# Kernel optimization log

Hardware: AMD Instinct MI355X
Metric: run time of the kernel (lower is better)

Reference implementation:

```python
import jax, jax.numpy as jnp
import numpy as np
import math

B, L, D_IN, H, N, NL, D_OUT = 16, 4096, 64, 256, 32, 4, 10
EPS = 1e-5


def setup_inputs() -> dict:
    key = jax.random.key(0)
    ks = jax.random.split(key, 16)
    inp = {}
    inp['x'] = jax.random.normal(ks[0], (B, L, D_IN), dtype=jnp.float32)
    inp['enc_w'] = jax.random.normal(ks[1], (H, D_IN), dtype=jnp.float32) / math.sqrt(D_IN)
    inp['enc_b'] = jax.random.normal(ks[2], (H,), dtype=jnp.float32) * 0.01
    # log_dt uniform in [log(1e-3), log(1e-1)] as in S4D init
    inp['log_dt'] = jax.random.uniform(ks[3], (NL, H), dtype=jnp.float32,
                                       minval=math.log(1e-3), maxval=math.log(1e-1))
    inp['log_A_real'] = jnp.full((NL, H, N), math.log(0.5), dtype=jnp.float32)
    inp['A_imag'] = jnp.broadcast_to(math.pi * jnp.arange(N, dtype=jnp.float32), (NL, H, N)).copy()
    inp['C_re'] = jax.random.normal(ks[4], (NL, H, N), dtype=jnp.float32)
    inp['C_im'] = jax.random.normal(ks[5], (NL, H, N), dtype=jnp.float32)
    inp['D'] = jax.random.normal(ks[6], (NL, H), dtype=jnp.float32)
    inp['out_w'] = jax.random.normal(ks[7], (NL, 2 * H, H), dtype=jnp.float32) / math.sqrt(H)
    inp['out_b'] = jax.random.normal(ks[8], (NL, 2 * H), dtype=jnp.float32) * 0.01
    inp['ln_w'] = jnp.ones((NL, H), dtype=jnp.float32)
    inp['ln_b'] = jnp.zeros((NL, H), dtype=jnp.float32)
    inp['dec_w'] = jax.random.normal(ks[9], (D_OUT, H), dtype=jnp.float32) / math.sqrt(H)
    inp['dec_b'] = jax.random.normal(ks[10], (D_OUT,), dtype=jnp.float32) * 0.01
    return inp


def _s4d_kernel(log_dt, log_A_real, A_imag, C_re, C_im, length):
    # log_dt: (H,), others: (H, N). Returns real conv kernel (H, length).
    dt = jnp.exp(log_dt)[:, None]                       # (H, 1)
    A = -jnp.exp(log_A_real) + 1j * A_imag              # (H, N), Re(A) < 0
    dtA = A * dt                                        # (H, N)
    C = (C_re + 1j * C_im) * (jnp.expm1(dtA)) / A       # ZOH-style scaling
    t = jnp.arange(length, dtype=jnp.float32)
    vand = jnp.exp(dtA[:, :, None] * t)                 # (H, N, L) Vandermonde
    K = 2.0 * jnp.real(jnp.einsum('hn,hnl->hl', C, vand))
    return K


def _fft_conv(u, k):
    # u: (B, H, L), k: (H, L) -> causal circular-padded conv, (B, H, L)
    length = u.shape[-1]
    k_f = jnp.fft.rfft(k, n=2 * length)                 # (H, L+1)
    u_f = jnp.fft.rfft(u, n=2 * length)                 # (B, H, L+1)
    return jnp.fft.irfft(u_f * k_f[None], n=2 * length)[..., :length]


def _layernorm_channels(x, w, b):
    # x: (B, H, L), normalize over channel dim H
    mu = jnp.mean(x, axis=1, keepdims=True)
    var = jnp.var(x, axis=1, keepdims=True)
    return (x - mu) * jax.lax.rsqrt(var + EPS) * w[None, :, None] + b[None, :, None]


def reference(x, enc_w, enc_b, log_dt, log_A_real, A_imag, C_re, C_im, D,
              out_w, out_b, ln_w, ln_b, dec_w, dec_b):
    # encoder: (B, L, d_input) -> (B, L, H), then transpose -> (B, H, L)
    h = jnp.einsum('bli,hi->blh', x, enc_w) + enc_b
    h = jnp.swapaxes(h, -1, -2)                         # (B, H, L)
    length = h.shape[-1]
    for i in range(NL):
        z = h
        K = _s4d_kernel(log_dt[i], log_A_real[i], A_imag[i], C_re[i], C_im[i], length)
        y = _fft_conv(z, K) + z * D[i][None, :, None]   # SSM conv + skip
        y = jax.nn.gelu(y)
        # position-wise 1x1 conv to 2H, then GLU over channel dim
        g = jnp.einsum('bhl,gh->bgl', y, out_w[i]) + out_b[i][None, :, None]
        g1, g2 = jnp.split(g, 2, axis=1)
        y = g1 * jax.nn.sigmoid(g2)
        h = y + h                                       # residual (dropout=0)
        h = _layernorm_channels(h, ln_w[i], ln_b[i])    # post-norm
    h = jnp.swapaxes(h, -1, -2)                         # (B, L, H)
    return jnp.einsum('blh,oh->blo', h, dec_w) + dec_b
```

## Files before the change

### kernel.cpp

```cpp
#include <hip/hip_runtime.h>
#include <hip/hip_fp16.h>

#define B_   16
#define L_   4096
#define DIN  64
#define H_   256
#define N_   32
#define NL_  4
#define DOUT 10
#define CH_  32
#define T_   128

#define GAS const __attribute__((address_space(1)))
#define LAS __attribute__((address_space(3)))

typedef _Float16 half8 __attribute__((ext_vector_type(8)));
typedef _Float16 half4 __attribute__((ext_vector_type(4)));
typedef float f32x4 __attribute__((ext_vector_type(4)));

__device__ __forceinline__ float gelu_f(float v) {
    float t3  = v * v * v;
    float arg = 0.7978845608028654f * fmaf(0.044715f, t3, v);
    float e   = __expf(2.f * arg);
    float th  = 1.f - 2.f / (e + 1.f);
    return 0.5f * v * (1.f + th);
}

__global__ __launch_bounds__(256) void gen_k(
    const float* __restrict__ log_dt, const float* __restrict__ log_A_real,
    const float* __restrict__ A_imag, const float* __restrict__ C_re, const float* __restrict__ C_im,
    const float* __restrict__ Dp,
    _Float16* __restrict__ Wv, _Float16* __restrict__ Vt, _Float16* __restrict__ G,
    float* __restrict__ wtr, float* __restrict__ wti)
{
    __shared__ float sxr[N_], sxi[N_], scr[N_], sci[N_], skd[T_];
    int ih = blockIdx.x;
    int t  = threadIdx.x;
    if (t < N_) {
        int n = t;
        float dt  = expf(log_dt[ih]);
        float Are = -expf(log_A_real[ih * N_ + n]);
        float Aim = A_imag[ih * N_ + n];
        float xr = dt * Are, xi = dt * Aim;
        float ex = expf(xr), cy = cosf(xi), sy = sinf(xi);
        float sh = sinf(0.5f * xi);
        float em_re = expm1f(xr) * cy - 2.f * sh * sh;
        float em_im = ex * sy;
        float inv = 1.f / (Are * Are + Aim * Aim);
        float qr = (em_re * Are + em_im * Aim) * inv;
        float qi = (em_im * Are - em_re * Aim) * inv;
        float crv = C_re[ih * N_ + n], civ = C_im[ih * N_ + n];
        sxr[n] = xr; sxi[n] = xi;
        scr[n] = 2.f * (crv * qr - civ * qi);
        sci[n] = 2.f * (crv * qi + civ * qr);
        float txr = 128.f * xr, txi = 128.f * xi;
        float exT = expf(txr);
        wtr[ih * N_ + n] = exT * cosf(txi);
        wti[ih * N_ + n] = exT * sinf(txi);
    }
    __syncthreads();
    if (t <= T_) {
        int d = t;
        float fd = (float)d;
        float kd = 0.f;
        for (int n = 0; n < N_; n++) {
            float ar = expf(fd * sxr[n]);
            float ang = fd * sxi[n];
            float wdr = ar * cosf(ang), wdi = ar * sinf(ang);
            if (d < T_) {
                kd = fmaf(scr[n], wdr, kd);
                kd = fmaf(-sci[n], wdi, kd);
                Wv[((size_t)ih * 64 + 2 * n) * T_ + (127 - d)]     = (_Float16)wdr;
                Wv[((size_t)ih * 64 + 2 * n + 1) * T_ + (127 - d)] = (_Float16)wdi;
            }
            if (d >= 1) {
                float vr = scr[n] * wdr - sci[n] * wdi;
                float vi = scr[n] * wdi + sci[n] * wdr;
                Vt[((size_t)ih * T_ + (d - 1)) * 64 + 2 * n]     = (_Float16)vr;
                Vt[((size_t)ih * T_ + (d - 1)) * 64 + 2 * n + 1] = (_Float16)(-vi);
            }
        }
        if (d < T_) skd[d] = kd;
    }
    __syncthreads();
    if (t < T_) {
        float v = skd[127 - t];
        if (t == 127) v += Dp[ih];
        G[(size_t)ih * 256 + t]       = (_Float16)v;
        G[(size_t)ih * 256 + 128 + t] = (_Float16)0.f;
    }
}

__global__ __launch_bounds__(256) void prep_k(
    const float* __restrict__ w, _Float16* __restrict__ w16,
    const float* __restrict__ dw, _Float16* __restrict__ dwp)
{
    int bx = blockIdx.x;
    int t  = threadIdx.x;
    if (bx < (NL_ * 2 * H_ * H_) / 256) {
        int idx = bx * 256 + t;
        w16[idx] = (_Float16)w[idx];
    } else {
#pragma unroll
        for (int j = 0; j < 16; j++) {
            int idx = j * 256 + t;
            dwp[idx] = (idx < DOUT * H_) ? (_Float16)dw[idx] : (_Float16)0.f;
        }
    }
}

__global__ __launch_bounds__(256) void encoder_k(
    const float* __restrict__ x, const float* __restrict__ ew,
    const float* __restrict__ eb, _Float16* __restrict__ z16)
{
    __shared__ _Float16 smem[35840];
    _Float16* xs  = smem;
    _Float16* ews = smem + 128 * 72;
    _Float16* ot  = smem;
    int b  = blockIdx.y;
    int l0 = blockIdx.x << 7;
    int t  = threadIdx.x;
#pragma unroll
    for (int j = 0; j < 8; j++) {
        int idx = j * 256 + t;
        int l = idx >> 4, i4 = (idx & 15) * 4;
        float4 v = *(const float4*)(x + ((size_t)(b * L_ + l0 + l)) * DIN + i4);
        _Float16 c[4] = {(_Float16)v.x, (_Float16)v.y, (_Float16)v.z, (_Float16)v.w};
        *(uint2*)&xs[l * 72 + i4] = *(uint2*)c;
    }
#pragma unroll
    for (int j = 0; j < 16; j++) {
        int idx = j * 256 + t;
        int h = idx >> 4, i4 = (idx & 15) * 4;
        float4 v = *(const float4*)(ew + h * 64 + i4);
        _Float16 c[4] = {(_Float16)v.x, (_Float16)v.y, (_Float16)v.z, (_Float16)v.w};
        *(uint2*)&ews[h * 72 + i4] = *(uint2*)c;
    }
    __syncthreads();
    int lane = t & 63, wid = t >> 6;
    int l15 = lane & 15, quad = lane >> 4;
    f32x4 acc[4][8];
#pragma unroll
    for (int mt = 0; mt < 4; mt++)
#pragma unroll
        for (int nt = 0; nt < 8; nt++) acc[mt][nt] = (f32x4){0.f,0.f,0.f,0.f};
#pragma unroll
    for (int ks = 0; ks < 2; ks++) {
        int kk = ks * 32 + quad * 8;
        half8 a[4], bb[8];
#pragma unroll
        for (int mt = 0; mt < 4; mt++)
            a[mt] = *(const half8*)&ews[(wid * 64 + mt * 16 + l15) * 72 + kk];
#pragma unroll
        for (int nt = 0; nt < 8; nt++)
            bb[nt] = *(const half8*)&xs[(nt * 16 + l15) * 72 + kk];
#pragma unroll
        for (int mt = 0; mt < 4; mt++)
#pragma unroll
            for (int nt = 0; nt < 8; nt++)
                acc[mt][nt] = __builtin_amdgcn_mfma_f32_16x16x32_f16(a[mt], bb[nt], acc[mt][nt], 0, 0, 0);
    }
    __syncthreads();
#pragma unroll
    for (int mt = 0; mt < 4; mt++) {
        int hb = wid * 64 + mt * 16 + quad * 4;
        float b0 = eb[hb], b1 = eb[hb + 1], b2 = eb[hb + 2], b3 = eb[hb + 3];
#pragma unroll
        for (int nt = 0; nt < 8; nt++) {
            int l = nt * 16 + l15;
            ot[(hb + 0) * 136 + l] = (_Float16)(acc[mt][nt][0] + b0);
            ot[(hb + 1) * 136 + l] = (_Float16)(acc[mt][nt][1] + b1);
            ot[(hb + 2) * 136 + l] = (_Float16)(acc[mt][nt][2] + b2);
            ot[(hb + 3) * 136 + l] = (_Float16)(acc[mt][nt][3] + b3);
        }
    }
    __syncthreads();
#pragma unroll
    for (int p = 0; p < 16; p++) {
        int row = p * 16 + (t >> 4), seg = t & 15;
        uint4 v = *(uint4*)&ot[row * 136 + seg * 8];
        *(uint4*)(z16 + ((size_t)(b * H_ + row)) * L_ + l0 + seg * 8) = v;
    }
}

__global__ __launch_bounds__(256, 4) void conv2_k(
    const _Float16* __restrict__ z16, const _Float16* __restrict__ G,
    const _Float16* __restrict__ Vt, const _Float16* __restrict__ Wv,
    const float* __restrict__ wtr, const float* __restrict__ wti,
    _Float16* __restrict__ y16)
{
    __shared__ _Float16 zT[64][136];
    __shared__ _Float16 Ff[64][72];
    __shared__ _Float16 Gs[256];
    int h = blockIdx.x, rb = blockIdx.y;
    int t = threadIdx.x;
    int b0 = rb * 2;
#pragma unroll
    for (int q = 0; q < 4; q++) {
        int idx = q * 256 + t;
        int brow = idx >> 9;
        int e = (idx & 511) * 8;
        uint4 v = *(const uint4*)(z16 + ((size_t)((b0 + brow) * H_ + h)) * L_ + e);
        int c = e >> 7, jj = e & 127;
        *(uint4*)&zT[brow * 32 + c][jj] = v;
    }
    Gs[t] = G[(size_t)h * 256 + t];
    __syncthreads();
    int lane = t & 63, w = t >> 6;
    int l15 = lane & 15, quad = lane >> 4;
    {
        int brow = w & 1, mhalf = w >> 1;
        f32x4 facc[2][2];
#pragma unroll
        for (int mt = 0; mt < 2; mt++) {
            facc[mt][0] = (f32x4){0.f,0.f,0.f,0.f};
            facc[mt][1] = (f32x4){0.f,0.f,0.f,0.f};
        }
        const _Float16* wvb = Wv + (size_t)h * 64 * T_;
#pragma unroll
        for (int ks = 0; ks < 4; ks++) {
            int kk = ks * 32 + quad * 8;
            half8 bf0 = *(const half8*)&zT[brow * 32 + l15][kk];
            half8 bf1 = *(const half8*)&zT[brow * 32 + 16 + l15][kk];
#pragma unroll
            for (int mt = 0; mt < 2; mt++) {
                half8 a = *(const half8*)(wvb + (size_t)((mhalf * 2 + mt) * 16 + l15) * T_ + kk);
                facc[mt][0] = __builtin_amdgcn_mfma_f32_16x16x32_f16(a, bf0, facc[mt][0], 0, 0, 0);
                facc[mt][1] = __builtin_amdgcn_mfma_f32_16x16x32_f16(a, bf1, facc[mt][1], 0, 0, 0);
            }
        }
#pragma unroll
        for (int mt = 0; mt < 2; mt++)
#pragma unroll
            for (int nt = 0; nt < 2; nt++) {
                int cr = brow * 32 + nt * 16 + l15;
                int cc = (mhalf * 2 + mt) * 16 + quad * 4;
#pragma unroll
                for (int r = 0; r < 4; r++)
                    Ff[cr][cc + r] = (_Float16)facc[mt][nt][r];
            }
    }
    __syncthreads();
    if (w < 2 && lane < 32) {
        int n = lane;
        float wr = wtr[h * N_ + n], wi = wti[h * N_ + n];
        float cr = 0.f, ci = 0.f;
        for (int c = 0; c < CH_; c++) {
            float fr = (float)Ff[w * 32 + c][2 * n];
            float fi = (float)Ff[w * 32 + c][2 * n + 1];
            Ff[w * 32 + c][2 * n]     = (_Float16)cr;
            Ff[w * 32 + c][2 * n + 1] = (_Float16)ci;
            float nr = fmaf(wr, cr, fr);
            nr = fmaf(-wi, ci, nr);
            float ni = fmaf(wi, cr, fi);
            ni = fmaf(wr, ci, ni);
            cr = nr; ci = ni;
        }
    }
    __syncthreads();
    f32x4 acc[2][4];
#pragma unroll
    for (int mt = 0; mt < 2; mt++)
#pragma unroll
        for (int nt = 0; nt < 4; nt++) acc[mt][nt] = (f32x4){0.f,0.f,0.f,0.f};
#pragma unroll
    for (int ks = 0; ks < 4; ks++) {
        int kk = ks * 32 + quad * 8;
        int base0 = 127 - (w * 32 + l15) + kk;
        int base1 = base0 - 16;
        half8 a0, a1;
#pragma unroll
        for (int j = 0; j < 8; j++) { a0[j] = Gs[base0 + j]; a1[j] = Gs[base1 + j]; }
#pragma unroll
        for (int nt = 0; nt < 4; nt++) {
            half8 bf = *(const half8*)&zT[nt * 16 + l15][kk];
            acc[0][nt] = __builtin_amdgcn_mfma_f32_16x16x32_f16(a0, bf, acc[0][nt], 0, 0, 0);
            acc[1][nt] = __builtin_amdgcn_mfma_f32_16x16x32_f16(a1, bf, acc[1][nt], 0, 0, 0);
        }
    }
    const _Float16* vb = Vt + (size_t)h * T_ * 64;
#pragma unroll
    for (int ks = 0; ks < 2; ks++) {
        int kk = ks * 32 + quad * 8;
        half8 a0 = *(const half8*)(vb + ((size_t)(w * 32 + l15)) * 64 + kk);
        half8 a1 = *(const half8*)(vb + ((size_t)(w * 32 + 16 + l15)) * 64 + kk);
#pragma unroll
        for (int nt = 0; nt < 4; nt++) {
            half8 bf = *(const half8*)&Ff[nt * 16 + l15][kk];
            acc[0][nt] = __builtin_amdgcn_mfma_f32_16x16x32_f16(a0, bf, acc[0][nt], 0, 0, 0);
            acc[1][nt] = __builtin_amdgcn_mfma_f32_16x16x32_f16(a1, bf, acc[1][nt], 0, 0, 0);
        }
    }
    __syncthreads();
#pragma unroll
    for (int mt = 0; mt < 2; mt++)
#pragma unroll
        for (int nt = 0; nt < 4; nt++) {
            int r = nt * 16 + l15;
            int tt0 = w * 32 + mt * 16 + quad * 4;
            _Float16 o[4];
#pragma unroll
            for (int rr = 0; rr < 4; rr++) o[rr] = (_Float16)gelu_f(acc[mt][nt][rr]);
            *(uint2*)&zT[r][tt0] = *(uint2*)o;
        }
    __syncthreads();
#pragma unroll
    for (int q = 0; q < 4; q++) {
        int idx = q * 256 + t;
        int brow = idx >> 9;
        int e = (idx & 511) * 8;
        int c = e >> 7, jj = e & 127;
        uint4 v = *(uint4*)&zT[brow * 32 + c][jj];
        *(uint4*)(y16 + ((size_t)((b0 + brow) * H_ + h)) * L_ + e) = v;
    }
}

__global__ __launch_bounds__(256, 2) void glu_k(
    const _Float16* __restrict__ W, const _Float16* __restrict__ y16,
    const float* __restrict__ outb, const float* __restrict__ lnw,
    const float* __restrict__ lnb, _Float16* __restrict__ z16)
{
    __shared__ __align__(16) _Float16 yT_u[64 * 266];
    __shared__ __align__(16) _Float16 zs[256 * 64];
    __shared__ float red[2][4][64];
    __shared__ float mus[64], rss[64];
    _Float16* yT = yT_u;
    _Float16* us = yT_u;
    int b  = blockIdx.y;
    int l0 = blockIdx.x << 6;
    int t  = threadIdx.x;
    int lane = t & 63, wid = t >> 6;
    int l15 = lane & 15, quad = lane >> 4;
    {
        const uint4* src = (const uint4*)(y16 + ((size_t)(b * H_ + t)) * L_ + l0);
        uint4 v[8];
#pragma unroll
        for (int j = 0; j < 8; j++) v[j] = src[j];
        {
            int rsub = lane >> 3, csub = (lane & 7) * 8;
#pragma unroll
            for (int q = 0; q < 8; q++) {
                int ch = wid * 64 + q * 8 + rsub;
                const _Float16* gp = z16 + ((size_t)(b * H_ + ch)) * L_ + l0 + csub;
                __builtin_amdgcn_global_load_lds((GAS unsigned*)(const void*)gp,
                                                 (LAS unsigned*)(void*)&zs[(wid * 64 + q * 8) * 64],
                                                 16, 0, 0);
            }
        }
        const _Float16* hv = (const _Float16*)v;
#pragma unroll
        for (int j = 0; j < 64; j++) yT[j * 266 + t] = hv[j];
    }
    __syncthreads();
    f32x4 acc[8][4];
#pragma unroll
    for (int mt = 0; mt < 8; mt++)
#pragma unroll
        for (int nt = 0; nt < 4; nt++) acc[mt][nt] = (f32x4){0.f,0.f,0.f,0.f};
#pragma unroll
    for (int ks = 0; ks < 8; ks++) {
        int kk = ks * 32 + quad * 8;
        half8 bf[4];
#pragma unroll
        for (int nt = 0; nt < 4; nt++) bf[nt] = *(const half8*)&yT[(nt * 16 + l15) * 266 + kk];
#pragma unroll
        for (int mt = 0; mt < 8; mt++) {
            int row = (mt >> 2) * 256 + wid * 64 + (mt & 3) * 16 + l15;
            half8 a = *(const half8*)(W + (size_t)row * H_ + kk);
#pragma unroll
            for (int nt = 0; nt < 4; nt++)
                acc[mt][nt] = __builtin_amdgcn_mfma_f32_16x16x32_f16(a, bf[nt], acc[mt][nt], 0, 0, 0);
        }
    }
    __syncthreads();
#pragma unroll
    for (int mt = 0; mt < 4; mt++) {
        int chb = wid * 64 + mt * 16 + quad * 4;
        float4 ob1 = *(const float4*)(outb + chb);
        float4 ob2 = *(const float4*)(outb + 256 + chb);
        const float* o1 = (const float*)&ob1;
        const float* o2 = (const float*)&ob2;
#pragma unroll
        for (int nt = 0; nt < 4; nt++) {
            int l = nt * 16 + l15;
#pragma unroll
            for (int r = 0; r < 4; r++) {
                float g1 = acc[mt][nt][r] + o1[r];
                float g2 = acc[mt + 4][nt][r] + o2[r];
                float sg = 1.f / (1.f + __expf(-g2));
                us[(chb + r) * 66 + l] = (_Float16)(g1 * sg);
            }
        }
    }
    __syncthreads();
    int lr = t & 63, grp = t >> 6;
    float s1 = 0.f, s2 = 0.f;
    for (int j = 0; j < 64; j++) {
        int ch = grp * 64 + j;
        float uu = (float)us[ch * 66 + lr] + (float)zs[ch * 64 + lr];
        us[ch * 66 + lr] = (_Float16)uu;
        s1 += uu; s2 = fmaf(uu, uu, s2);
    }
    red[0][grp][lr] = s1; red[1][grp][lr] = s2;
    __syncthreads();
    if (t < 64) {
        float a = red[0][0][t] + red[0][1][t] + red[0][2][t] + red[0][3][t];
        float q = red[1][0][t] + red[1][1][t] + red[1][2][t] + red[1][3][t];
        float mu  = a * (1.f / 256.f);
        float var = q * (1.f / 256.f) - mu * mu;
        mus[t] = mu; rss[t] = rsqrtf(var + 1e-5f);
    }
    __syncthreads();
    int lg = (t & 15) * 4, ch0 = t >> 4;
    float mu4[4], rs4[4];
#pragma unroll
    for (int i = 0; i < 4; i++) { mu4[i] = mus[lg + i]; rs4[i] = rss[lg + i]; }
#pragma unroll
    for (int j = 0; j < 16; j++) {
        int ch = ch0 + 16 * j;
        float wv = lnw[ch], bv = lnb[ch];
        _Float16 o4[4];
#pragma unroll
        for (int i = 0; i < 4; i++) {
            float vv = ((float)us[ch * 66 + lg + i] - mu4[i]) * rs4[i] * wv + bv;
            o4[i] = (_Float16)vv;
        }
        *(uint2*)(z16 + ((size_t)(b * H_ + ch)) * L_ + l0 + lg) = *(uint2*)o4;
    }
}

__global__ __launch_bounds__(256) void decoder_k(
    const _Float16* __restrict__ z16, const _Float16* __restrict__ dwp,
    const float* __restrict__ db, float* __restrict__ out)
{
    __shared__ _Float16 zT[128][268];
    int b  = blockIdx.y;
    int l0 = blockIdx.x << 7;
    int t  = threadIdx.x;
#pragma unroll 8
    for (int j = 0; j < 64; j++) {
        int idx = j * 256 + t;
        int h = idx >> 6, lp = idx & 63;
        unsigned v = *(const unsigned*)(z16 + ((size_t)(b * H_ + h)) * L_ + l0 + lp * 2);
        union { unsigned u; _Float16 f[2]; } c; c.u = v;
        zT[lp * 2][h]     = c.f[0];
        zT[lp * 2 + 1][h] = c.f[1];
    }
    __syncthreads();
    int lane = t & 63, wid = t >> 6;
    int l15 = lane & 15, quad = lane >> 4;
    f32x4 acc[2];
    acc[0] = (f32x4){0.f,0.f,0.f,0.f};
    acc[1] = (f32x4){0.f,0.f,0.f,0.f};
#pragma unroll
    for (int ks = 0; ks < 8; ks++) {
        int kk = ks * 32 + quad * 8;
        half8 a = *(const half8*)(dwp + l15 * 256 + kk);
#pragma unroll
        for (int nt = 0; nt < 2; nt++) {
            int l = (wid * 2 + nt) * 16 + l15;
            half4 lo = *(const half4*)&zT[l][kk];
            half4 hi = *(const half4*)&zT[l][kk + 4];
            half8 bf;
#pragma unroll
            for (int j = 0; j < 4; j++) { bf[j] = lo[j]; bf[j + 4] = hi[j]; }
            acc[nt] = __builtin_amdgcn_mfma_f32_16x16x32_f16(a, bf, acc[nt], 0, 0, 0);
        }
    }
    int o0 = quad * 4;
#pragma unroll
    for (int nt = 0; nt < 2; nt++) {
        int l = (wid * 2 + nt) * 16 + l15;
        float* op = out + ((size_t)(b * L_ + l0 + l)) * DOUT;
#pragma unroll
        for (int r = 0; r < 4; r++) {
            int o = o0 + r;
            if (o < DOUT) op[o] = acc[nt][r] + db[o];
        }
    }
}

extern "C" void kernel_launch(void* const* d_in, const int* in_sizes, int n_in,
                              void* d_out, int out_size, void* d_ws, size_t ws_size,
                              hipStream_t stream)
{
    (void)in_sizes; (void)n_in; (void)out_size; (void)ws_size;
    const float* x          = (const float*)d_in[0];
    const float* enc_w      = (const float*)d_in[1];
    const float* enc_b      = (const float*)d_in[2];
    const float* log_dt     = (const float*)d_in[3];
    const float* log_A_real = (const float*)d_in[4];
    const float* A_imag     = (const float*)d_in[5];
    const float* C_re       = (const float*)d_in[6];
    const float* C_im       = (const float*)d_in[7];
    const float* Dp         = (const float*)d_in[8];
    const float* out_w      = (const float*)d_in[9];
    const float* out_b      = (const float*)d_in[10];
    const float* ln_w       = (const float*)d_in[11];
    const float* ln_b       = (const float*)d_in[12];
    const float* dec_w      = (const float*)d_in[13];
    const float* dec_b      = (const float*)d_in[14];
    float* outp = (float*)d_out;

    char* ws = (char*)d_ws;
    _Float16* z16 = (_Float16*)ws;   ws += (size_t)B_ * H_ * L_ * 2;
    _Float16* y16 = (_Float16*)ws;   ws += (size_t)B_ * H_ * L_ * 2;
    _Float16* Wv = (_Float16*)ws;    ws += (size_t)NL_ * H_ * 64 * T_ * 2;
    _Float16* Vt = (_Float16*)ws;    ws += (size_t)NL_ * H_ * T_ * 64 * 2;
    _Float16* G  = (_Float16*)ws;    ws += (size_t)NL_ * H_ * 256 * 2;
    size_t tb = (size_t)NL_ * H_ * N_;
    float* wtr = (float*)ws; ws += tb * 4;
    float* wti = (float*)ws; ws += tb * 4;
    _Float16* W16 = (_Float16*)ws; ws += (size_t)NL_ * 2 * H_ * H_ * 2;
    _Float16* dwp = (_Float16*)ws; ws += (size_t)16 * H_ * 2;

    gen_k<<<NL_ * H_, 256, 0, stream>>>(log_dt, log_A_real, A_imag, C_re, C_im, Dp,
                                        Wv, Vt, G, wtr, wti);
    prep_k<<<(NL_ * 2 * H_ * H_) / 256 + 1, 256, 0, stream>>>(out_w, W16, dec_w, dwp);
    encoder_k<<<dim3(L_ / 128, B_), 256, 0, stream>>>(x, enc_w, enc_b, z16);
    for (int i = 0; i < NL_; i++) {
        size_t th = (size_t)i * H_;
        conv2_k<<<dim3(H_, B_ / 2), 256, 0, stream>>>(z16, G + th * 256, Vt + th * T_ * 64,
                                                      Wv + th * 64 * T_, wtr + th * N_, wti + th * N_,
                                                      y16);
        glu_k<<<dim3(L_ / 64, B_), 256, 0, stream>>>(W16 + (size_t)i * 2 * H_ * H_, y16,
                                                     out_b + i * 2 * H_, ln_w + th, ln_b + th, z16);
    }
    decoder_k<<<dim3(L_ / 128, B_), 256, 0, stream>>>(z16, dwp, dec_b, outp);
}
```

Measured before the change: 518.1 us.

## Fuse encoder, layer loop and decoder into one persistent kernel with grid barriers

Replaces the chain of encoder, per-layer conv and GLU, and decoder launches with a single persistent kernel of 512 blocks. Stages are separated by atomic-counter grid barriers, and each block loops over virtual tiles inside a stage. The fp16 weight conversion moves into gen_k, which removes the separate prep kernel. The aim is to cut launch gaps and per-kernel tail effects. In exchange it relies on all 512 blocks being co-resident (launch bounds of 2 blocks per CU with 72KB of shared memory), and forces a fixed grid and fixed occupancy on every stage.

New measurement: 2.011 ms. 288% more time.

```diff
diff --git a/kernel.cpp b/kernel.cpp
--- a/kernel.cpp
+++ b/kernel.cpp
@@ -10,6 +10,7 @@
 #define DOUT 10
 #define CH_  32
 #define T_   128
+#define NBLK 512
 
 #define GAS const __attribute__((address_space(1)))
 #define LAS __attribute__((address_space(3)))
@@ -26,16 +27,48 @@
     return 0.5f * v * (1.f + th);
 }
 
+__device__ __forceinline__ void gbar(int* bar, int phase) {
+    __syncthreads();
+    if (threadIdx.x == 0) {
+        int* cnt = bar + phase * 32;
+        int* flg = bar + phase * 32 + 16;
+        __threadfence();
+        int v = __hip_atomic_fetch_add(cnt, 1, __ATOMIC_ACQ_REL, __HIP_MEMORY_SCOPE_AGENT);
+        if (v == NBLK - 1) {
+            __hip_atomic_store(flg, 1, __ATOMIC_RELEASE, __HIP_MEMORY_SCOPE_AGENT);
+        } else {
+            while (!__hip_atomic_load(flg, __ATOMIC_ACQUIRE, __HIP_MEMORY_SCOPE_AGENT))
+                __builtin_amdgcn_s_sleep(2);
+        }
+        __threadfence();
+    }
+    __syncthreads();
+}
+
 __global__ __launch_bounds__(256) void gen_k(
     const float* __restrict__ log_dt, const float* __restrict__ log_A_real,
     const float* __restrict__ A_imag, const float* __restrict__ C_re, const float* __restrict__ C_im,
     const float* __restrict__ Dp,
     _Float16* __restrict__ Wv, _Float16* __restrict__ Vt, _Float16* __restrict__ G,
-    float* __restrict__ wtr, float* __restrict__ wti)
+    float* __restrict__ wtr, float* __restrict__ wti,
+    const float* __restrict__ outw, _Float16* __restrict__ w16,
+    const float* __restrict__ dw, _Float16* __restrict__ dwp)
 {
     __shared__ float sxr[N_], sxi[N_], scr[N_], sci[N_], skd[T_];
     int ih = blockIdx.x;
     int t  = threadIdx.x;
+    {
+        int base = ih * 512 + t;
+        w16[base]       = (_Float16)outw[base];
+        w16[base + 256] = (_Float16)outw[base + 256];
+    }
+    if (ih == 0) {
+#pragma unroll
+        for (int j = 0; j < 16; j++) {
+            int idx = j * 256 + t;
+            dwp[idx] = (idx < DOUT * H_) ? (_Float16)dw[idx] : (_Float16)0.f;
+        }
+    }
     if (t < N_) {
         int n = t;
         float dt  = expf(log_dt[ih]);
@@ -91,391 +124,390 @@
     }
 }
 
-__global__ __launch_bounds__(256) void prep_k(
-    const float* __restrict__ w, _Float16* __restrict__ w16,
-    const float* __restrict__ dw, _Float16* __restrict__ dwp)
+__global__ __launch_bounds__(256, 2) void fused_k(
+    const float* __restrict__ x, const float* __restrict__ ew, const float* __restrict__ eb,
+    const _Float16* __restrict__ G, const _Float16* __restrict__ Vt, const _Float16* __restrict__ Wv,
+    const float* __restrict__ wtr, const float* __restrict__ wti,
+    const _Float16* __restrict__ W16, const float* __restrict__ outb,
+    const float* __restrict__ lnw, const float* __restrict__ lnb,
+    const _Float16* __restrict__ dwp, const float* __restrict__ db,
+    _Float16* __restrict__ z16, _Float16* __restrict__ y16,
+    float* __restrict__ outp, int* bar)
 {
-    int bx = blockIdx.x;
-    int t  = threadIdx.x;
-    if (bx < (NL_ * 2 * H_ * H_) / 256) {
-        int idx = bx * 256 + t;
-        w16[idx] = (_Float16)w[idx];
-    } else {
-#pragma unroll
-        for (int j = 0; j < 16; j++) {
-            int idx = j * 256 + t;
-            dwp[idx] = (idx < DOUT * H_) ? (_Float16)dw[idx] : (_Float16)0.f;
-        }
-    }
-}
-
-__global__ __launch_bounds__(256) void encoder_k(
-    const float* __restrict__ x, const float* __restrict__ ew,
-    const float* __restrict__ eb, _Float16* __restrict__ z16)
-{
-    __shared__ _Float16 smem[35840];
-    _Float16* xs  = smem;
-    _Float16* ews = smem + 128 * 72;
-    _Float16* ot  = smem;
-    int b  = blockIdx.y;
-    int l0 = blockIdx.x << 7;
-    int t  = threadIdx.x;
-#pragma unroll
-    for (int j = 0; j < 8; j++) {
-        int idx = j * 256 + t;
-        int l = idx >> 4, i4 = (idx & 15) * 4;
-        float4 v = *(const float4*)(x + ((size_t)(b * L_ + l0 + l)) * DIN + i4);
-        _Float16 c[4] = {(_Float16)v.x, (_Float16)v.y, (_Float16)v.z, (_Float16)v.w};
-        *(uint2*)&xs[l * 72 + i4] = *(uint2*)c;
-    }
-#pragma unroll
-    for (int j = 0; j < 16; j++) {
-        int idx = j * 256 + t;
-        int h = idx >> 4, i4 = (idx & 15) * 4;
-        float4 v = *(const float4*)(ew + h * 64 + i4);
-        _Float16 c[4] = {(_Float16)v.x, (_Float16)v.y, (_Float16)v.z, (_Float16)v.w};
-        *(uint2*)&ews[h * 72 + i4] = *(uint2*)c;
-    }
-    __syncthreads();
-    int lane = t & 63, wid = t >> 6;
-    int l15 = lane & 15, quad = lane >> 4;
-    f32x4 acc[4][8];
-#pragma unroll
-    for (int mt = 0; mt < 4; mt++)
-#pragma unroll
-        for (int nt = 0; nt < 8; nt++) acc[mt][nt] = (f32x4){0.f,0.f,0.f,0.f};
-#pragma unroll
-    for (int ks = 0; ks < 2; ks++) {
-        int kk = ks * 32 + quad * 8;
-        half8 a[4], bb[8];
-#pragma unroll
-        for (int mt = 0; mt < 4; mt++)
-            a[mt] = *(const half8*)&ews[(wid * 64 + mt * 16 + l15) * 72 + kk];
-#pragma unroll
-        for (int nt = 0; nt < 8; nt++)
-            bb[nt] = *(const half8*)&xs[(nt * 16 + l15) * 72 + kk];
-#pragma unroll
-        for (int mt = 0; mt < 4; mt++)
-#pragma unroll
-            for (int nt = 0; nt < 8; nt++)
-                acc[mt][nt] = __builtin_amdgcn_mfma_f32_16x16x32_f16(a[mt], bb[nt], acc[mt][nt], 0, 0, 0);
-    }
-    __syncthreads();
-#pragma unroll
-    for (int mt = 0; mt < 4; mt++) {
-        int hb = wid * 64 + mt * 16 + quad * 4;
-        float b0 = eb[hb], b1 = eb[hb + 1], b2 = eb[hb + 2], b3 = eb[hb + 3];
-#pragma unroll
-        for (int nt = 0; nt < 8; nt++) {
-            int l = nt * 16 + l15;
-            ot[(hb + 0) * 136 + l] = (_Float16)(acc[mt][nt][0] + b0);
-            ot[(hb + 1) * 136 + l] = (_Float16)(acc[mt][nt][1] + b1);
-            ot[(hb + 2) * 136 + l] = (_Float16)(acc[mt][nt][2] + b2);
-            ot[(hb + 3) * 136 + l] = (_Float16)(acc[mt][nt][3] + b3);
-        }
-    }
-    __syncthreads();
-#pragma unroll
-    for (int p = 0; p < 16; p++) {
-        int row = p * 16 + (t >> 4), seg = t & 15;
-        uint4 v = *(uint4*)&ot[row * 136 + seg * 8];
-        *(uint4*)(z16 + ((size_t)(b * H_ + row)) * L_ + l0 + seg * 8) = v;
-    }
-}
-
-__global__ __launch_bounds__(256, 4) void conv2_k(
-    const _Float16* __restrict__ z16, const _Float16* __restrict__ G,
-    const _Float16* __restrict__ Vt, const _Float16* __restrict__ Wv,
-    const float* __restrict__ wtr, const float* __restrict__ wti,
-    _Float16* __restrict__ y16)
-{
-    __shared__ _Float16 zT[64][136];
-    __shared__ _Float16 Ff[64][72];
-    __shared__ _Float16 Gs[256];
-    int h = blockIdx.x, rb = blockIdx.y;
-    int t = threadIdx.x;
-    int b0 = rb * 2;
-#pragma unroll
-    for (int q = 0; q < 4; q++) {
-        int idx = q * 256 + t;
-        int brow = idx >> 9;
-        int e = (idx & 511) * 8;
-        uint4 v = *(const uint4*)(z16 + ((size_t)((b0 + brow) * H_ + h)) * L_ + e);
-        int c = e >> 7, jj = e & 127;
-        *(uint4*)&zT[brow * 32 + c][jj] = v;
-    }
-    Gs[t] = G[(size_t)h * 256 + t];
-    __syncthreads();
-    int lane = t & 63, w = t >> 6;
-    int l15 = lane & 15, quad = lane >> 4;
-    {
-        int brow = w & 1, mhalf = w >> 1;
-        f32x4 facc[2][2];
-#pragma unroll
-        for (int mt = 0; mt < 2; mt++) {
-            facc[mt][0] = (f32x4){0.f,0.f,0.f,0.f};
-            facc[mt][1] = (f32x4){0.f,0.f,0.f,0.f};
-        }
-        const _Float16* wvb = Wv + (size_t)h * 64 * T_;
-#pragma unroll
-        for (int ks = 0; ks < 4; ks++) {
-            int kk = ks * 32 + quad * 8;
-            half8 bf0 = *(const half8*)&zT[brow * 32 + l15][kk];
-            half8 bf1 = *(const half8*)&zT[brow * 32 + 16 + l15][kk];
-#pragma unroll
-            for (int mt = 0; mt < 2; mt++) {
-                half8 a = *(const half8*)(wvb + (size_t)((mhalf * 2 + mt) * 16 + l15) * T_ + kk);
-                facc[mt][0] = __builtin_amdgcn_mfma_f32_16x16x32_f16(a, bf0, facc[mt][0], 0, 0, 0);
-                facc[mt][1] = __builtin_amdgcn_mfma_f32_16x16x32_f16(a, bf1, facc[mt][1], 0, 0, 0);
-            }
-        }
-#pragma unroll
-        for (int mt = 0; mt < 2; mt++)
-#pragma unroll
-            for (int nt = 0; nt < 2; nt++) {
-                int cr = brow * 32 + nt * 16 + l15;
-                int cc = (mhalf * 2 + mt) * 16 + quad * 4;
-#pragma unroll
-                for (int r = 0; r < 4; r++)
-                    Ff[cr][cc + r] = (_Float16)facc[mt][nt][r];
-            }
-    }
-    __syncthreads();
-    if (w < 2 && lane < 32) {
-        int n = lane;
-        float wr = wtr[h * N_ + n], wi = wti[h * N_ + n];
-        float cr = 0.f, ci = 0.f;
-        for (int c = 0; c < CH_; c++) {
-            float fr = (float)Ff[w * 32 + c][2 * n];
-            float fi = (float)Ff[w * 32 + c][2 * n + 1];
-            Ff[w * 32 + c][2 * n]     = (_Float16)cr;
-            Ff[w * 32 + c][2 * n + 1] = (_Float16)ci;
-            float nr = fmaf(wr, cr, fr);
-            nr = fmaf(-wi, ci, nr);
-            float ni = fmaf(wi, cr, fi);
-            ni = fmaf(wr, ci, ni);
-            cr = nr; ci = ni;
-        }
-    }
-    __syncthreads();
-    f32x4 acc[2][4];
-#pragma unroll
-    for (int mt = 0; mt < 2; mt++)
-#pragma unroll
-        for (int nt = 0; nt < 4; nt++) acc[mt][nt] = (f32x4){0.f,0.f,0.f,0.f};
-#pragma unroll
-    for (int ks = 0; ks < 4; ks++) {
-        int kk = ks * 32 + quad * 8;
-        int base0 = 127 - (w * 32 + l15) + kk;
-        int base1 = base0 - 16;
-        half8 a0, a1;
-#pragma unroll
-        for (int j = 0; j < 8; j++) { a0[j] = Gs[base0 + j]; a1[j] = Gs[base1 + j]; }
-#pragma unroll
-        for (int nt = 0; nt < 4; nt++) {
-            half8 bf = *(const half8*)&zT[nt * 16 + l15][kk];
-            acc[0][nt] = __builtin_amdgcn_mfma_f32_16x16x32_f16(a0, bf, acc[0][nt], 0, 0, 0);
-            acc[1][nt] = __builtin_amdgcn_mfma_f32_16x16x32_f16(a1, bf, acc[1][nt], 0, 0, 0);
-        }
-    }
-    const _Float16* vb = Vt + (size_t)h * T_ * 64;
-#pragma unroll
-    for (int ks = 0; ks < 2; ks++) {
-        int kk = ks * 32 + quad * 8;
-        half8 a0 = *(const half8*)(vb + ((size_t)(w * 32 + l15)) * 64 + kk);
-        half8 a1 = *(const half8*)(vb + ((size_t)(w * 32 + 16 + l15)) * 64 + kk);
-#pragma unroll
-        for (int nt = 0; nt < 4; nt++) {
-            half8 bf = *(const half8*)&Ff[nt * 16 + l15][kk];
-            acc[0][nt] = __builtin_amdgcn_mfma_f32_16x16x32_f16(a0, bf, acc[0][nt], 0, 0, 0);
-            acc[1][nt] = __builtin_amdgcn_mfma_f32_16x16x32_f16(a1, bf, acc[1][nt], 0, 0, 0);
-        }
-    }
-    __syncthreads();
-#pragma unroll
-    for (int mt = 0; mt < 2; mt++)
-#pragma unroll
-        for (int nt = 0; nt < 4; nt++) {
-            int r = nt * 16 + l15;
-            int tt0 = w * 32 + mt * 16 + quad * 4;
-            _Float16 o[4];
-#pragma unroll
-            for (int rr = 0; rr < 4; rr++) o[rr] = (_Float16)gelu_f(acc[mt][nt][rr]);
-            *(uint2*)&zT[r][tt0] = *(uint2*)o;
-        }
-    __syncthreads();
-#pragma unroll
-    for (int q = 0; q < 4; q++) {
-        int idx = q * 256 + t;
-        int brow = idx >> 9;
-        int e = (idx & 511) * 8;
-        int c = e >> 7, jj = e & 127;
-        uint4 v = *(uint4*)&zT[brow * 32 + c][jj];
-        *(uint4*)(y16 + ((size_t)((b0 + brow) * H_ + h)) * L_ + e) = v;
-    }
-}
-
-__global__ __launch_bounds__(256, 2) void glu_k(
-    const _Float16* __restrict__ W, const _Float16* __restrict__ y16,
-    const float* __restrict__ outb, const float* __restrict__ lnw,
-    const float* __restrict__ lnb, _Float16* __restrict__ z16)
-{
-    __shared__ __align__(16) _Float16 yT_u[64 * 266];
-    __shared__ __align__(16) _Float16 zs[256 * 64];
-    __shared__ float red[2][4][64];
-    __shared__ float mus[64], rss[64];
-    _Float16* yT = yT_u;
-    _Float16* us = yT_u;
-    int b  = blockIdx.y;
-    int l0 = blockIdx.x << 6;
+    __shared__ __align__(16) char smem[73728];
     int t  = threadIdx.x;
     int lane = t & 63, wid = t >> 6;
     int l15 = lane & 15, quad = lane >> 4;
+    int ph = 0;
+
     {
-        const uint4* src = (const uint4*)(y16 + ((size_t)(b * H_ + t)) * L_ + l0);
-        uint4 v[8];
-#pragma unroll
-        for (int j = 0; j < 8; j++) v[j] = src[j];
+        _Float16* xs  = (_Float16*)smem;
+        _Float16* ews = (_Float16*)(smem + 18432);
+        _Float16* ot  = (_Float16*)smem;
+        int vid = blockIdx.x;
+        int b  = vid >> 5;
+        int l0 = (vid & 31) << 7;
+#pragma unroll
+        for (int j = 0; j < 8; j++) {
+            int idx = j * 256 + t;
+            int l = idx >> 4, i4 = (idx & 15) * 4;
+            float4 v = *(const float4*)(x + ((size_t)(b * L_ + l0 + l)) * DIN + i4);
+            _Float16 c[4] = {(_Float16)v.x, (_Float16)v.y, (_Float16)v.z, (_Float16)v.w};
+            *(uint2*)&xs[l * 72 + i4] = *(uint2*)c;
+        }
+#pragma unroll
+        for (int j = 0; j < 16; j++) {
+            int idx = j * 256 + t;
+            int h = idx >> 4, i4 = (idx & 15) * 4;
+            float4 v = *(const float4*)(ew + h * 64 + i4);
+            _Float16 c[4] = {(_Float16)v.x, (_Float16)v.y, (_Float16)v.z, (_Float16)v.w};
+            *(uint2*)&ews[h * 72 + i4] = *(uint2*)c;
+        }
+        __syncthreads();
+        f32x4 acc[4][8];
+#pragma unroll
+        for (int mt = 0; mt < 4; mt++)
+#pragma unroll
+            for (int nt = 0; nt < 8; nt++) acc[mt][nt] = (f32x4){0.f,0.f,0.f,0.f};
+#pragma unroll
+        for (int ks = 0; ks < 2; ks++) {
+            int kk = ks * 32 + quad * 8;
+            half8 a[4], bb[8];
+#pragma unroll
+            for (int mt = 0; mt < 4; mt++)
+                a[mt] = *(const half8*)&ews[(wid * 64 + mt * 16 + l15) * 72 + kk];
+#pragma unroll
+            for (int nt = 0; nt < 8; nt++)
+                bb[nt] = *(const half8*)&xs[(nt * 16 + l15) * 72 + kk];
+#pragma unroll
+            for (int mt = 0; mt < 4; mt++)
+#pragma unroll
+                for (int nt = 0; nt < 8; nt++)
+                    acc[mt][nt] = __builtin_amdgcn_mfma_f32_16x16x32_f16(a[mt], bb[nt], acc[mt][nt], 0, 0, 0);
+        }
+        __syncthreads();
+#pragma unroll
+        for (int mt = 0; mt < 4; mt++) {
+            int hb = wid * 64 + mt * 16 + quad * 4;
+            float b0 = eb[hb], b1 = eb[hb + 1], b2 = eb[hb + 2], b3 = eb[hb + 3];
+#pragma unroll
+            for (int nt = 0; nt < 8; nt++) {
+                int l = nt * 16 + l15;
+                ot[(hb + 0) * 136 + l] = (_Float16)(acc[mt][nt][0] + b0);
+                ot[(hb + 1) * 136 + l] = (_Float16)(acc[mt][nt][1] + b1);
+                ot[(hb + 2) * 136 + l] = (_Float16)(acc[mt][nt][2] + b2);
+                ot[(hb + 3) * 136 + l] = (_Float16)(acc[mt][nt][3] + b3);
+            }
+        }
+        __syncthreads();
+#pragma unroll
+        for (int p = 0; p < 16; p++) {
+            int row = p * 16 + (t >> 4), seg = t & 15;
+            uint4 v = *(uint4*)&ot[row * 136 + seg * 8];
+            *(uint4*)(z16 + ((size_t)(b * H_ + row)) * L_ + l0 + seg * 8) = v;
+        }
+    }
+    gbar(bar, ph++);
+
+    for (int i = 0; i < NL_; i++) {
+        const _Float16* Gl  = G  + (size_t)i * H_ * 256;
+        const _Float16* Vtl = Vt + (size_t)i * H_ * T_ * 64;
+        const _Float16* Wvl = Wv + (size_t)i * H_ * 64 * T_;
+        const float* wtrl = wtr + (size_t)i * H_ * N_;
+        const float* wtil = wti + (size_t)i * H_ * N_;
+        const _Float16* Wl = W16 + (size_t)i * 2 * H_ * H_;
+        const float* obl = outb + i * 2 * H_;
+        const float* lwl = lnw + i * H_;
+        const float* lbl = lnb + i * H_;
+
         {
-            int rsub = lane >> 3, csub = (lane & 7) * 8;
-#pragma unroll
-            for (int q = 0; q < 8; q++) {
-                int ch = wid * 64 + q * 8 + rsub;
-                const _Float16* gp = z16 + ((size_t)(b * H_ + ch)) * L_ + l0 + csub;
-                __builtin_amdgcn_global_load_lds((GAS unsigned*)(const void*)gp,
-                                                 (LAS unsigned*)(void*)&zs[(wid * 64 + q * 8) * 64],
-                                                 16, 0, 0);
-            }
-        }
-        const _Float16* hv = (const _Float16*)v;
-#pragma unroll
-        for (int j = 0; j < 64; j++) yT[j * 266 + t] = hv[j];
-    }
-    __syncthreads();
-    f32x4 acc[8][4];
-#pragma unroll
-    for (int mt = 0; mt < 8; mt++)
-#pragma unroll
-        for (int nt = 0; nt < 4; nt++) acc[mt][nt] = (f32x4){0.f,0.f,0.f,0.f};
-#pragma unroll
-    for (int ks = 0; ks < 8; ks++) {
-        int kk = ks * 32 + quad * 8;
-        half8 bf[4];
-#pragma unroll
-        for (int nt = 0; nt < 4; nt++) bf[nt] = *(const half8*)&yT[(nt * 16 + l15) * 266 + kk];
-#pragma unroll
-        for (int mt = 0; mt < 8; mt++) {
-            int row = (mt >> 2) * 256 + wid * 64 + (mt & 3) * 16 + l15;
-            half8 a = *(const half8*)(W + (size_t)row * H_ + kk);
-#pragma unroll
-            for (int nt = 0; nt < 4; nt++)
-                acc[mt][nt] = __builtin_amdgcn_mfma_f32_16x16x32_f16(a, bf[nt], acc[mt][nt], 0, 0, 0);
-        }
-    }
-    __syncthreads();
-#pragma unroll
-    for (int mt = 0; mt < 4; mt++) {
-        int chb = wid * 64 + mt * 16 + quad * 4;
-        float4 ob1 = *(const float4*)(outb + chb);
-        float4 ob2 = *(const float4*)(outb + 256 + chb);
-        const float* o1 = (const float*)&ob1;
-        const float* o2 = (const float*)&ob2;
-#pragma unroll
-        for (int nt = 0; nt < 4; nt++) {
-            int l = nt * 16 + l15;
-#pragma unroll
-            for (int r = 0; r < 4; r++) {
-                float g1 = acc[mt][nt][r] + o1[r];
-                float g2 = acc[mt + 4][nt][r] + o2[r];
-                float sg = 1.f / (1.f + __expf(-g2));
-                us[(chb + r) * 66 + l] = (_Float16)(g1 * sg);
-            }
-        }
-    }
-    __syncthreads();
-    int lr = t & 63, grp = t >> 6;
-    float s1 = 0.f, s2 = 0.f;
-    for (int j = 0; j < 64; j++) {
-        int ch = grp * 64 + j;
-        float uu = (float)us[ch * 66 + lr] + (float)zs[ch * 64 + lr];
-        us[ch * 66 + lr] = (_Float16)uu;
-        s1 += uu; s2 = fmaf(uu, uu, s2);
-    }
-    red[0][grp][lr] = s1; red[1][grp][lr] = s2;
-    __syncthreads();
-    if (t < 64) {
-        float a = red[0][0][t] + red[0][1][t] + red[0][2][t] + red[0][3][t];
-        float q = red[1][0][t] + red[1][1][t] + red[1][2][t] + red[1][3][t];
-        float mu  = a * (1.f / 256.f);
-        float var = q * (1.f / 256.f) - mu * mu;
-        mus[t] = mu; rss[t] = rsqrtf(var + 1e-5f);
-    }
-    __syncthreads();
-    int lg = (t & 15) * 4, ch0 = t >> 4;
-    float mu4[4], rs4[4];
-#pragma unroll
-    for (int i = 0; i < 4; i++) { mu4[i] = mus[lg + i]; rs4[i] = rss[lg + i]; }
-#pragma unroll
-    for (int j = 0; j < 16; j++) {
-        int ch = ch0 + 16 * j;
-        float wv = lnw[ch], bv = lnb[ch];
-        _Float16 o4[4];
-#pragma unroll
-        for (int i = 0; i < 4; i++) {
-            float vv = ((float)us[ch * 66 + lg + i] - mu4[i]) * rs4[i] * wv + bv;
-            o4[i] = (_Float16)vv;
-        }
-        *(uint2*)(z16 + ((size_t)(b * H_ + ch)) * L_ + l0 + lg) = *(uint2*)o4;
-    }
-}
-
-__global__ __launch_bounds__(256) void decoder_k(
-    const _Float16* __restrict__ z16, const _Float16* __restrict__ dwp,
-    const float* __restrict__ db, float* __restrict__ out)
-{
-    __shared__ _Float16 zT[128][268];
-    int b  = blockIdx.y;
-    int l0 = blockIdx.x << 7;
-    int t  = threadIdx.x;
+            _Float16* zT = (_Float16*)smem;
+            _Float16* Ff = (_Float16*)(smem + 17408);
+            _Float16* Gs = (_Float16*)(smem + 26624);
+            for (int v2 = blockIdx.x; v2 < 2048; v2 += NBLK) {
+                int h = v2 & 255, rb = v2 >> 8;
+                int b0 = rb * 2;
+#pragma unroll
+                for (int q = 0; q < 4; q++) {
+                    int idx = q * 256 + t;
+                    int brow = idx >> 9;
+                    int e = (idx & 511) * 8;
+                    uint4 v = *(const uint4*)(z16 + ((size_t)((b0 + brow) * H_ + h)) * L_ + e);
+                    int c = e >> 7, jj = e & 127;
+                    *(uint4*)&zT[(brow * 32 + c) * 136 + jj] = v;
+                }
+                Gs[t] = Gl[(size_t)h * 256 + t];
+                __syncthreads();
+                {
+                    int brow = wid & 1, mhalf = wid >> 1;
+                    f32x4 facc[2][2];
+#pragma unroll
+                    for (int mt = 0; mt < 2; mt++) {
+                        facc[mt][0] = (f32x4){0.f,0.f,0.f,0.f};
+                        facc[mt][1] = (f32x4){0.f,0.f,0.f,0.f};
+                    }
+                    const _Float16* wvb = Wvl + (size_t)h * 64 * T_;
+#pragma unroll
+                    for (int ks = 0; ks < 4; ks++) {
+                        int kk = ks * 32 + quad * 8;
+                        half8 bf0 = *(const half8*)&zT[(brow * 32 + l15) * 136 + kk];
+                        half8 bf1 = *(const half8*)&zT[(brow * 32 + 16 + l15) * 136 + kk];
+#pragma unroll
+                        for (int mt = 0; mt < 2; mt++) {
+                            half8 a = *(const half8*)(wvb + (size_t)((mhalf * 2 + mt) * 16 + l15) * T_ + kk);
+                            facc[mt][0] = __builtin_amdgcn_mfma_f32_16x16x32_f16(a, bf0, facc[mt][0], 0, 0, 0);
+                            facc[mt][1] = __builtin_amdgcn_mfma_f32_16x16x32_f16(a, bf1, facc[mt][1], 0, 0, 0);
+                        }
+                    }
+#pragma unroll
+                    for (int mt = 0; mt < 2; mt++)
+#pragma unroll
+                        for (int nt = 0; nt < 2; nt++) {
+                            int cr = brow * 32 + nt * 16 + l15;
+                            int cc = (mhalf * 2 + mt) * 16 + quad * 4;
+#pragma unroll
+                            for (int r = 0; r < 4; r++)
+                                Ff[cr * 72 + cc + r] = (_Float16)facc[mt][nt][r];
+                        }
+                }
+                __syncthreads();
+                if (wid < 2 && lane < 32) {
+                    int n = lane;
+                    float wr = wtrl[h * N_ + n], wi = wtil[h * N_ + n];
+                    float cr = 0.f, ci = 0.f;
+                    for (int c = 0; c < CH_; c++) {
+                        float fr = (float)Ff[(wid * 32 + c) * 72 + 2 * n];
+                        float fi = (float)Ff[(wid * 32 + c) * 72 + 2 * n + 1];
+                        Ff[(wid * 32 + c) * 72 + 2 * n]     = (_Float16)cr;
+                        Ff[(wid * 32 + c) * 72 + 2 * n + 1] = (_Float16)ci;
+                        float nr = fmaf(wr, cr, fr);
+                        nr = fmaf(-wi, ci, nr);
+                        float ni = fmaf(wi, cr, fi);
+                        ni = fmaf(wr, ci, ni);
+                        cr = nr; ci = ni;
+                    }
+                }
+                __syncthreads();
+                f32x4 acc[2][4];
+#pragma unroll
+                for (int mt = 0; mt < 2; mt++)
+#pragma unroll
+                    for (int nt = 0; nt < 4; nt++) acc[mt][nt] = (f32x4){0.f,0.f,0.f,0.f};
+#pragma unroll
+                for (int ks = 0; ks < 4; ks++) {
+                    int kk = ks * 32 + quad * 8;
+                    int base0 = 127 - (wid * 32 + l15) + kk;
+                    int base1 = base0 - 16;
+                    half8 a0, a1;
+#pragma unroll
+                    for (int j = 0; j < 8; j++) { a0[j] = Gs[base0 + j]; a1[j] = Gs[base1 + j]; }
+#pragma unroll
+                    for (int nt = 0; nt < 4; nt++) {
+                        half8 bf = *(const half8*)&zT[(nt * 16 + l15) * 136 + kk];
+                        acc[0][nt] = __builtin_amdgcn_mfma_f32_16x16x32_f16(a0, bf, acc[0][nt], 0, 0, 0);
+                        acc[1][nt] = __builtin_amdgcn_mfma_f32_16x16x32_f16(a1, bf, acc[1][nt], 0, 0, 0);
+                    }
+                }
+                const _Float16* vb = Vtl + (size_t)h * T_ * 64;
+#pragma unroll
+                for (int ks = 0; ks < 2; ks++) {
+                    int kk = ks * 32 + quad * 8;
+                    half8 a0 = *(const half8*)(vb + ((size_t)(wid * 32 + l15)) * 64 + kk);
+                    half8 a1 = *(const half8*)(vb + ((size_t)(wid * 32 + 16 + l15)) * 64 + kk);
+#pragma unroll
+                    for (int nt = 0; nt < 4; nt++) {
+                        half8 bf = *(const half8*)&Ff[(nt * 16 + l15) * 72 + kk];
+                        acc[0][nt] = __builtin_amdgcn_mfma_f32_16x16x32_f16(a0, bf, acc[0][nt], 0, 0, 0);
+                        acc[1][nt] = __builtin_amdgcn_mfma_f32_16x16x32_f16(a1, bf, acc[1][nt], 0, 0, 0);
+                    }
+                }
+                __syncthreads();
+#pragma unroll
+                for (int mt = 0; mt < 2; mt++)
+#pragma unroll
+                    for (int nt = 0; nt < 4; nt++) {
+                        int r = nt * 16 + l15;
+                        int tt0 = wid * 32 + mt * 16 + quad * 4;
+                        _Float16 o[4];
+#pragma unroll
+                        for (int rr = 0; rr < 4; rr++) o[rr] = (_Float16)gelu_f(acc[mt][nt][rr]);
+                        *(uint2*)&zT[r * 136 + tt0] = *(uint2*)o;
+                    }
+                __syncthreads();
+#pragma unroll
+                for (int q = 0; q < 4; q++) {
+                    int idx = q * 256 + t;
+                    int brow = idx >> 9;
+                    int e = (idx & 511) * 8;
+                    int c = e >> 7, jj = e & 127;
+                    uint4 v = *(uint4*)&zT[(brow * 32 + c) * 136 + jj];
+                    *(uint4*)(y16 + ((size_t)((b0 + brow) * H_ + h)) * L_ + e) = v;
+                }
+                __syncthreads();
+            }
+        }
+        gbar(bar, ph++);
+
+        {
+            _Float16* yT  = (_Float16*)smem;
+            _Float16* us  = (_Float16*)smem;
+            _Float16* zs  = (_Float16*)(smem + 34048);
+            float* red    = (float*)(smem + 66816);
+            float* mus    = (float*)(smem + 68864);
+            float* rss    = (float*)(smem + 69120);
+            for (int v2 = blockIdx.x; v2 < 1024; v2 += NBLK) {
+                int b  = v2 >> 6;
+                int l0 = (v2 & 63) << 6;
+                {
+                    const uint4* src = (const uint4*)(y16 + ((size_t)(b * H_ + t)) * L_ + l0);
+                    uint4 v[8];
+#pragma unroll
+                    for (int j = 0; j < 8; j++) v[j] = src[j];
+                    {
+                        int rsub = lane >> 3, csub = (lane & 7) * 8;
+#pragma unroll
+                        for (int q = 0; q < 8; q++) {
+                            int ch = wid * 64 + q * 8 + rsub;
+                            const _Float16* gp = z16 + ((size_t)(b * H_ + ch)) * L_ + l0 + csub;
+                            __builtin_amdgcn_global_load_lds((GAS unsigned*)(const void*)gp,
+                                                             (LAS unsigned*)(void*)&zs[(wid * 64 + q * 8) * 64],
+                                                             16, 0, 0);
+                        }
+                    }
+                    const _Float16* hv = (const _Float16*)v;
+#pragma unroll
+                    for (int j = 0; j < 64; j++) yT[j * 266 + t] = hv[j];
+                }
+                __syncthreads();
+                f32x4 acc[8][4];
+#pragma unroll
+                for (int mt = 0; mt < 8; mt++)
+#pragma unroll
+                    for (int nt = 0; nt < 4; nt++) acc[mt][nt] = (f32x4){0.f,0.f,0.f,0.f};
+#pragma unroll
+                for (int ks = 0; ks < 8; ks++) {
+                    int kk = ks * 32 + quad * 8;
+                    half8 bf[4];
+#pragma unroll
+                    for (int nt = 0; nt < 4; nt++) bf[nt] = *(const half8*)&yT[(nt * 16 + l15) * 266 + kk];
+#pragma unroll
+                    for (int mt = 0; mt < 8; mt++) {
+                        int row = (mt >> 2) * 256 + wid * 64 + (mt & 3) * 16 + l15;
+                        half8 a = *(const half8*)(Wl + (size_t)row * H_ + kk);
+#pragma unroll
+                        for (int nt = 0; nt < 4; nt++)
+                            acc[mt][nt] = __builtin_amdgcn_mfma_f32_16x16x32_f16(a, bf[nt], acc[mt][nt], 0, 0, 0);
+                    }
+                }
+                __syncthreads();
+#pragma unroll
+                for (int mt = 0; mt < 4; mt++) {
+                    int chb = wid * 64 + mt * 16 + quad * 4;
+                    float4 ob1 = *(const float4*)(obl + chb);
+                    float4 ob2 = *(const float4*)(obl + 256 + chb);
+                    const float* o1 = (const float*)&ob1;
+                    const float* o2 = (const float*)&ob2;
+#pragma unroll
+                    for (int nt = 0; nt < 4; nt++) {
+                        int l = nt * 16 + l15;
+#pragma unroll
+                        for (int r = 0; r < 4; r++) {
+                            float g1 = acc[mt][nt][r] + o1[r];
+                            float g2 = acc[mt + 4][nt][r] + o2[r];
+                            float sg = 1.f / (1.f + __expf(-g2));
+                            us[(chb + r) * 66 + l] = (_Float16)(g1 * sg);
+                        }
+                    }
+                }
+                __syncthreads();
+                {
+                    int lr = t & 63, grp = t >> 6;
+                    float s1 = 0.f, s2 = 0.f;
+                    for (int j = 0; j < 64; j++) {
+                        int ch = grp * 64 + j;
+                        float uu = (float)us[ch * 66 + lr] + (float)zs[ch * 64 + lr];
+                        us[ch * 66 + lr] = (_Float16)uu;
+                        s1 += uu; s2 = fmaf(uu, uu, s2);
+                    }
+                    red[(0 * 4 + grp) * 64 + lr] = s1;
+                    red[(1 * 4 + grp) * 64 + lr] = s2;
+                }
+                __syncthreads();
+                if (t < 64) {
+                    float a = red[0*256 + 0*64 + t] + red[0*256 + 1*64 + t] + red[0*256 + 2*64 + t] + red[0*256 + 3*64 + t];
+                    float q = red[1*256 + 0*64 + t] + red[1*256 + 1*64 + t] + red[1*256 + 2*64 + t] + red[1*256 + 3*64 + t];
+                    float mu  = a * (1.f / 256.f);
+                    float var = q * (1.f / 256.f) - mu * mu;
+                    mus[t] = mu; rss[t] = rsqrtf(var + 1e-5f);
+                }
+                __syncthreads();
+                {
+                    int lg = (t & 15) * 4, ch0 = t >> 4;
+                    float mu4[4], rs4[4];
+#pragma unroll
+                    for (int i2 = 0; i2 < 4; i2++) { mu4[i2] = mus[lg + i2]; rs4[i2] = rss[lg + i2]; }
+#pragma unroll
+                    for (int j = 0; j < 16; j++) {
+                        int ch = ch0 + 16 * j;
+                        float wv = lwl[ch], bv = lbl[ch];
+                        _Float16 o4[4];
+#pragma unroll
+                        for (int i2 = 0; i2 < 4; i2++) {
+                            float vv = ((float)us[ch * 66 + lg + i2] - mu4[i2]) * rs4[i2] * wv + bv;
+                            o4[i2] = (_Float16)vv;
+                        }
+                        *(uint2*)(z16 + ((size_t)(b * H_ + ch)) * L_ + l0 + lg) = *(uint2*)o4;
+                    }
+                }
+                __syncthreads();
+            }
+        }
+        gbar(bar, ph++);
+    }
+
+    {
+        _Float16* zT = (_Float16*)smem;
+        int vid = blockIdx.x;
+        int b  = vid >> 5;
+        int l0 = (vid & 31) << 7;
 #pragma unroll 8
-    for (int j = 0; j < 64; j++) {
-        int idx = j * 256 + t;
-        int h = idx >> 6, lp = idx & 63;
-        unsigned v = *(const unsigned*)(z16 + ((size_t)(b * H_ + h)) * L_ + l0 + lp * 2);
-        union { unsigned u; _Float16 f[2]; } c; c.u = v;
-        zT[lp * 2][h]     = c.f[0];
-        zT[lp * 2 + 1][h] = c.f[1];
-    }
-    __syncthreads();
-    int lane = t & 63, wid = t >> 6;
-    int l15 = lane & 15, quad = lane >> 4;
-    f32x4 acc[2];
-    acc[0] = (f32x4){0.f,0.f,0.f,0.f};
-    acc[1] = (f32x4){0.f,0.f,0.f,0.f};
-#pragma unroll
-    for (int ks = 0; ks < 8; ks++) {
-        int kk = ks * 32 + quad * 8;
-        half8 a = *(const half8*)(dwp + l15 * 256 + kk);
+        for (int j = 0; j < 64; j++) {
+            int idx = j * 256 + t;
+            int h = idx >> 6, lp = idx & 63;
+            unsigned v = *(const unsigned*)(z16 + ((size_t)(b * H_ + h)) * L_ + l0 + lp * 2);
+            union { unsigned u; _Float16 f[2]; } c; c.u = v;
+            zT[(lp * 2) * 268 + h]     = c.f[0];
+            zT[(lp * 2 + 1) * 268 + h] = c.f[1];
+        }
+        __syncthreads();
+        f32x4 acc[2];
+        acc[0] = (f32x4){0.f,0.f,0.f,0.f};
+        acc[1] = (f32x4){0.f,0.f,0.f,0.f};
+#pragma unroll
+        for (int ks = 0; ks < 8; ks++) {
+            int kk = ks * 32 + quad * 8;
+            half8 a = *(const half8*)(dwp + l15 * 256 + kk);
+#pragma unroll
+            for (int nt = 0; nt < 2; nt++) {
+                int l = (wid * 2 + nt) * 16 + l15;
+                half4 lo = *(const half4*)&zT[l * 268 + kk];
+                half4 hi = *(const half4*)&zT[l * 268 + kk + 4];
+                half8 bf;
+#pragma unroll
+                for (int j = 0; j < 4; j++) { bf[j] = lo[j]; bf[j + 4] = hi[j]; }
+                acc[nt] = __builtin_amdgcn_mfma_f32_16x16x32_f16(a, bf, acc[nt], 0, 0, 0);
+            }
+        }
+        int o0 = quad * 4;
 #pragma unroll
         for (int nt = 0; nt < 2; nt++) {
             int l = (wid * 2 + nt) * 16 + l15;
-            half4 lo = *(const half4*)&zT[l][kk];
-            half4 hi = *(const half4*)&zT[l][kk + 4];
-            half8 bf;
-#pragma unroll
-            for (int j = 0; j < 4; j++) { bf[j] = lo[j]; bf[j + 4] = hi[j]; }
-            acc[nt] = __builtin_amdgcn_mfma_f32_16x16x32_f16(a, bf, acc[nt], 0, 0, 0);
-        }
-    }
-    int o0 = quad * 4;
-#pragma unroll
-    for (int nt = 0; nt < 2; nt++) {
-        int l = (wid * 2 + nt) * 16 + l15;
-        float* op = out + ((size_t)(b * L_ + l0 + l)) * DOUT;
-#pragma unroll
-        for (int r = 0; r < 4; r++) {
-            int o = o0 + r;
-            if (o < DOUT) op[o] = acc[nt][r] + db[o];
+            float* op = outp + ((size_t)(b * L_ + l0 + l)) * DOUT;
+#pragma unroll
+            for (int r = 0; r < 4; r++) {
+                int o = o0 + r;
+                if (o < DOUT) op[o] = acc[nt][r] + db[o];
+            }
         }
     }
 }
@@ -513,18 +545,12 @@
     float* wti = (float*)ws; ws += tb * 4;
     _Float16* W16 = (_Float16*)ws; ws += (size_t)NL_ * 2 * H_ * H_ * 2;
     _Float16* dwp = (_Float16*)ws; ws += (size_t)16 * H_ * 2;
-
+    int* bar = (int*)ws; ws += 4096;
+
+    hipMemsetAsync(bar, 0, 4096, stream);
     gen_k<<<NL_ * H_, 256, 0, stream>>>(log_dt, log_A_real, A_imag, C_re, C_im, Dp,
-                                        Wv, Vt, G, wtr, wti);
-    prep_k<<<(NL_ * 2 * H_ * H_) / 256 + 1, 256, 0, stream>>>(out_w, W16, dec_w, dwp);
-    encoder_k<<<dim3(L_ / 128, B_), 256, 0, stream>>>(x, enc_w, enc_b, z16);
-    for (int i = 0; i < NL_; i++) {
-        size_t th = (size_t)i * H_;
-        conv2_k<<<dim3(H_, B_ / 2), 256, 0, stream>>>(z16, G + th * 256, Vt + th * T_ * 64,
-                                                      Wv + th * 64 * T_, wtr + th * N_, wti + th * N_,
-                                                      y16);
-        glu_k<<<dim3(L_ / 64, B_), 256, 0, stream>>>(W16 + (size_t)i * 2 * H_ * H_, y16,
-                                                     out_b + i * 2 * H_, ln_w + th, ln_b + th, z16);
-    }
-    decoder_k<<<dim3(L_ / 128, B_), 256, 0, stream>>>(z16, dwp, dec_b, outp);
+                                        Wv, Vt, G, wtr, wti, out_w, W16, dec_w, dwp);
+    fused_k<<<NBLK, 256, 0, stream>>>(x, enc_w, enc_b, G, Vt, Wv, wtr, wti,
+                                      W16, out_b, ln_w, ln_b, dwp, dec_b,
+                                      z16, y16, outp, bar);
 }
```
